# Optimization experiments

Measured on AMD Instinct MI355X. Metric: run time of the kernel, lower is better.

Reference implementation:

```python
import jax, jax.numpy as jnp
import numpy as np

Y_SCALE = 0.01  # fixed weight quantization scale (q_scale of the int8 weights)


def setup_inputs() -> dict:
    key = jax.random.key(0)
    kx, kw, kb = jax.random.split(key, 3)
    B, S, IN, OUT = 4, 2048, 4096, 4096
    x = jax.random.normal(kx, (B, S, IN), dtype=jnp.float32)
    # int8 quantized weights, stored transposed as (in_features, out_features)
    weight_q = jax.random.randint(kw, (IN, OUT), -128, 128, dtype=jnp.int32)
    bias = jax.random.normal(kb, (OUT,), dtype=jnp.float32)
    return {"x": x, "weight_q": weight_q, "bias": bias}


def reference(x, weight_q, bias):
    # Per-batch-sample dynamic activation scale: max(|x_i|)/128 over each [S, IN] slice
    x_scale = jnp.max(jnp.abs(x), axis=(1, 2), keepdims=True) / 128.0  # [B,1,1]
    # int8 quantize: round + clip
    xq = jnp.clip(jnp.round(x / x_scale), -128, 127).astype(jnp.int8)  # [B,S,IN]
    wq = weight_q.astype(jnp.int8)                                      # [IN,OUT]
    c = jax.lax.dot_general(
        xq, wq,
        dimension_numbers=(((2,), (0,)), ((), ())),
        preferred_element_type=jnp.int32,
    )  # [B,S,OUT]
    # dequantize and bias-add
    y = c.astype(jnp.float32) * (x_scale * Y_SCALE)
    return y + bias
```

## Files before the change

kernel.cpp:

```cpp
#include <hip/hip_runtime.h>
#include <stdint.h>

#define K_DIM 4096
#define N_DIM 4096
#define M_DIM 8192
#define S_ROWS 2048
#define NT 32

typedef int v4i __attribute__((ext_vector_type(4)));

__device__ __forceinline__ void gload16(const void* g, void* l) {
    __builtin_amdgcn_global_load_lds(
        (const __attribute__((address_space(1))) unsigned int*)g,
        (__attribute__((address_space(3))) unsigned int*)l, 16, 0, 0);
}

__device__ __forceinline__ void barrier() {
    asm volatile("" ::: "memory");
    __builtin_amdgcn_s_barrier();
    asm volatile("" ::: "memory");
}

__global__ void absmax_kernel(const float* __restrict__ x, unsigned* __restrict__ amax) {
    int b = blockIdx.y;
    const float4* xb = (const float4*)(x + (size_t)b * S_ROWS * K_DIM);
    int tid = blockIdx.x * 256 + threadIdx.x;
    const int stride = 1024 * 256;
    float m = 0.f;
#pragma unroll
    for (int i = 0; i < 8; ++i) {
        float4 v = xb[tid + i * stride];
        m = fmaxf(m, fmaxf(fmaxf(fabsf(v.x), fabsf(v.y)),
                           fmaxf(fabsf(v.z), fabsf(v.w))));
    }
#pragma unroll
    for (int off = 32; off; off >>= 1)
        m = fmaxf(m, __shfl_xor(m, off));
    __shared__ float red[4];
    if ((threadIdx.x & 63) == 0) red[threadIdx.x >> 6] = m;
    __syncthreads();
    if (threadIdx.x == 0) {
        m = fmaxf(fmaxf(red[0], red[1]), fmaxf(red[2], red[3]));
        atomicMax(&amax[b], __float_as_uint(m));
    }
}

__global__ void quant_kernel(const float* __restrict__ x,
                             const unsigned* __restrict__ amax,
                             char* __restrict__ xq) {
    size_t gid = (size_t)blockIdx.x * 256 + threadIdx.x;
    size_t base = gid * 16;
    int b = (int)(base >> 23);
    float inv = 128.0f / __uint_as_float(amax[b]);
    const float4* xs = (const float4*)(x + base);
    unsigned parts[4];
#pragma unroll
    for (int i = 0; i < 4; ++i) {
        float4 v = xs[i];
        int q0 = max(-128, min(127, (int)rintf(v.x * inv)));
        int q1 = max(-128, min(127, (int)rintf(v.y * inv)));
        int q2 = max(-128, min(127, (int)rintf(v.z * inv)));
        int q3 = max(-128, min(127, (int)rintf(v.w * inv)));
        parts[i] = (q0 & 255) | ((q1 & 255) << 8) | ((q2 & 255) << 16) | ((q3 & 255) << 24);
    }
    *(uint4*)(xq + base) = make_uint4(parts[0], parts[1], parts[2], parts[3]);
}

__global__ void wtrans_kernel(const int* __restrict__ wq, char* __restrict__ wt) {
    __shared__ unsigned lds[64 * 17];
    int t = threadIdx.x;
    int c = t & 63;
    int g = t >> 6;
    int n0 = blockIdx.x * 64;
    int k0 = blockIdx.y * 64;
#pragma unroll
    for (int rep = 0; rep < 4; ++rep) {
        int kb = g * 16 + rep * 4;
        int v0 = wq[(size_t)(k0 + kb + 0) * N_DIM + n0 + c];
        int v1 = wq[(size_t)(k0 + kb + 1) * N_DIM + n0 + c];
        int v2 = wq[(size_t)(k0 + kb + 2) * N_DIM + n0 + c];
        int v3 = wq[(size_t)(k0 + kb + 3) * N_DIM + n0 + c];
        lds[c * 17 + (kb >> 2)] =
            (v0 & 255) | ((v1 & 255) << 8) | ((v2 & 255) << 16) | ((v3 & 255) << 24);
    }
    __syncthreads();
    int row = t >> 2;
    int ch = t & 3;
    uint4 o;
    o.x = lds[row * 17 + ch * 4 + 0];
    o.y = lds[row * 17 + ch * 4 + 1];
    o.z = lds[row * 17 + ch * 4 + 2];
    o.w = lds[row * 17 + ch * 4 + 3];
    *(uint4*)(wt + (size_t)(n0 + row) * K_DIM + k0 + ch * 16) = o;
}

__global__ __launch_bounds__(512, 2) void gemm8_kernel(
    const char* __restrict__ A, const char* __restrict__ Bt,
    const float* __restrict__ bias, const unsigned* __restrict__ amax,
    float* __restrict__ out) {
    __shared__ char sm[131072];
    const int t = threadIdx.x;
    const int l = t & 63;
    const int w = t >> 6;
    const int wm = w >> 2;
    const int wn = w & 3;
    const int rb = l & 15;
    const int sg = l >> 4;

    int bid = blockIdx.x;
    int swz = (bid & 7) * 64 + (bid >> 3);
    int mt = swz >> 4, nt = swz & 15;
    const size_t m0 = (size_t)mt * 256;
    const size_t n0 = (size_t)nt * 256;

    v4i acc[8][4];
#pragma unroll
    for (int i = 0; i < 8; ++i)
#pragma unroll
        for (int j = 0; j < 4; ++j) acc[i][j] = (v4i){0, 0, 0, 0};

#define ST_A(tt, h)                                                          \
    if ((tt) < NT) {                                                         \
        char* lb = sm + (((tt) & 1) * 65536);                                \
        const char* gb = A + m0 * K_DIM + (size_t)(tt) * 128;                \
        _Pragma("unroll")                                                    \
        for (int j = 0; j < 2; ++j) {                                        \
            int p = j * 512 + t;                                             \
            int r7 = p >> 3, sl = p & 7;                                     \
            int r = (r7 & 63) + ((r7 >> 6) << 7) + ((h) << 6);               \
            int s = sl ^ (r & 7);                                            \
            gload16(gb + (size_t)r * K_DIM + s * 16, lb + r * 128 + sl * 16);\
        }                                                                    \
    }
#define ST_B(tt, h)                                                          \
    if ((tt) < NT) {                                                         \
        char* lb = sm + (((tt) & 1) * 65536) + 32768;                        \
        const char* gb = Bt + n0 * K_DIM + (size_t)(tt) * 128;               \
        _Pragma("unroll")                                                    \
        for (int j = 0; j < 2; ++j) {                                        \
            int p = j * 512 + t;                                             \
            int r7 = p >> 3, sl = p & 7;                                     \
            int r = ((r7 >> 5) << 6) + ((h) << 5) + (r7 & 31);               \
            int s = sl ^ (r & 7);                                            \
            gload16(gb + (size_t)r * K_DIM + s * 16, lb + r * 128 + sl * 16);\
        }                                                                    \
    }

    ST_A(0, 0); ST_B(0, 0); ST_A(0, 1); ST_B(0, 1); ST_A(1, 0); ST_B(1, 0);

    v4i aF[4][2], bL[2][2], bH[2][2];

    for (int i = 0; i < NT; ++i) {
        const char* pA = sm + (i & 1) * 65536;
        const char* pB = pA + 32768;
        if (i == NT - 1) { asm volatile("s_waitcnt vmcnt(0)" ::: "memory"); }
        else             { asm volatile("s_waitcnt vmcnt(4)" ::: "memory"); }
        barrier();

#pragma unroll
        for (int mi = 0; mi < 4; ++mi)
#pragma unroll
            for (int ks = 0; ks < 2; ++ks) {
                int r = wm * 128 + mi * 16 + rb;
                aF[mi][ks] = *(const v4i*)(pA + r * 128 + (((ks << 2) + sg) ^ (r & 7)) * 16);
            }
#pragma unroll
        for (int ni = 0; ni < 2; ++ni)
#pragma unroll
            for (int ks = 0; ks < 2; ++ks) {
                int r = wn * 64 + ni * 16 + rb;
                bL[ni][ks] = *(const v4i*)(pB + r * 128 + (((ks << 2) + sg) ^ (r & 7)) * 16);
            }
        ST_A(i + 1, 1);
        ST_B(i + 1, 1);
        __builtin_amdgcn_s_setprio(1);
#pragma unroll
        for (int mi = 0; mi < 4; ++mi)
#pragma unroll
            for (int ni = 0; ni < 2; ++ni)
#pragma unroll
                for (int ks = 0; ks < 2; ++ks)
                    acc[mi][ni] = __builtin_amdgcn_mfma_i32_16x16x64_i8(
                        aF[mi][ks], bL[ni][ks], acc[mi][ni], 0, 0, 0);
#pragma unroll
        for (int ni = 0; ni < 2; ++ni)
#pragma unroll
            for (int ks = 0; ks < 2; ++ks) {
                int r = wn * 64 + 32 + ni * 16 + rb;
                bH[ni][ks] = *(const v4i*)(pB + r * 128 + (((ks << 2) + sg) ^ (r & 7)) * 16);
            }
#pragma unroll
        for (int mi = 0; mi < 4; ++mi)
#pragma unroll
            for (int ni = 0; ni < 2; ++ni)
#pragma unroll
                for (int ks = 0; ks < 2; ++ks)
                    acc[mi][ni + 2] = __builtin_amdgcn_mfma_i32_16x16x64_i8(
                        aF[mi][ks], bH[ni][ks], acc[mi][ni + 2], 0, 0, 0);
        __builtin_amdgcn_s_setprio(0);
        barrier();

#pragma unroll
        for (int mi = 0; mi < 4; ++mi)
#pragma unroll
            for (int ks = 0; ks < 2; ++ks) {
                int r = wm * 128 + 64 + mi * 16 + rb;
                aF[mi][ks] = *(const v4i*)(pA + r * 128 + (((ks << 2) + sg) ^ (r & 7)) * 16);
            }
        ST_A(i + 2, 0);
        ST_B(i + 2, 0);
        __builtin_amdgcn_s_setprio(1);
#pragma unroll
        for (int mi = 0; mi < 4; ++mi)
#pragma unroll
            for (int ni = 0; ni < 2; ++ni)
#pragma unroll
                for (int ks = 0; ks < 2; ++ks)
                    acc[mi + 4][ni + 2] = __builtin_amdgcn_mfma_i32_16x16x64_i8(
                        aF[mi][ks], bH[ni][ks], acc[mi + 4][ni + 2], 0, 0, 0);
#pragma unroll
        for (int mi = 0; mi < 4; ++mi)
#pragma unroll
            for (int ni = 0; ni < 2; ++ni)
#pragma unroll
                for (int ks = 0; ks < 2; ++ks)
                    acc[mi + 4][ni] = __builtin_amdgcn_mfma_i32_16x16x64_i8(
                        aF[mi][ks], bL[ni][ks], acc[mi + 4][ni], 0, 0, 0);
        __builtin_amdgcn_s_setprio(0);
    }

    float scale = __uint_as_float(amax[m0 >> 11]) * (1.0f / 128.0f) * 0.01f;
    float bv[4];
#pragma unroll
    for (int ni = 0; ni < 4; ++ni) bv[ni] = bias[n0 + wn * 64 + ni * 16 + rb];
#pragma unroll
    for (int mi = 0; mi < 8; ++mi) {
#pragma unroll
        for (int rg = 0; rg < 4; ++rg) {
            size_t row = m0 + wm * 128 + mi * 16 + sg * 4 + rg;
            float* orow = out + row * N_DIM + n0 + wn * 64 + rb;
#pragma unroll
            for (int ni = 0; ni < 4; ++ni)
                orow[ni * 16] = (float)acc[mi][ni][rg] * scale + bv[ni];
        }
    }
#undef ST_A
#undef ST_B
}

extern "C" void kernel_launch(void* const* d_in, const int* in_sizes, int n_in,
                              void* d_out, int out_size, void* d_ws, size_t ws_size,
                              hipStream_t stream) {
    const float* x = (const float*)d_in[0];
    const int* wq = (const int*)d_in[1];
    const float* bias = (const float*)d_in[2];
    float* out = (float*)d_out;

    unsigned* amax = (unsigned*)d_ws;
    char* xq = (char*)d_ws + 256;
    char* wt = (char*)d_ws + 256 + (size_t)M_DIM * K_DIM;

    hipMemsetAsync(d_ws, 0, 16, stream);

    wtrans_kernel<<<dim3(64, 64), 256, 0, stream>>>(wq, wt);
    absmax_kernel<<<dim3(1024, 4), 256, 0, stream>>>(x, amax);
    quant_kernel<<<8192, 256, 0, stream>>>(x, amax, xq);
    gemm8_kernel<<<dim3(512), 512, 0, stream>>>(xq, wt, bias, amax, out);
}
```

Before: 228.5 us.

## Merge absmax and weight transpose kernels; simplify GEMM to single-stage double buffer

Combines the activation absmax and the weight transpose into one launch, with the block index picking the role, so one kernel launch and its tail gap go away. The GEMM main loop drops the split half-tile prefetch with vmcnt(4) and instead issues a full next-tile load once per iteration behind a vmcnt(0) wait. It also precomputes the swizzled LDS offsets, loads all B fragments at once and removes one barrier per iteration. This cuts barriers and address math, but it weakens the overlap of global loads with compute and holds more fragment registers live.

```diff
diff --git a/kernel.cpp b/kernel.cpp
--- a/kernel.cpp
+++ b/kernel.cpp
@@ -21,27 +21,58 @@
     asm volatile("" ::: "memory");
 }
 
-__global__ void absmax_kernel(const float* __restrict__ x, unsigned* __restrict__ amax) {
-    int b = blockIdx.y;
-    const float4* xb = (const float4*)(x + (size_t)b * S_ROWS * K_DIM);
-    int tid = blockIdx.x * 256 + threadIdx.x;
-    const int stride = 1024 * 256;
-    float m = 0.f;
-#pragma unroll
-    for (int i = 0; i < 8; ++i) {
-        float4 v = xb[tid + i * stride];
-        m = fmaxf(m, fmaxf(fmaxf(fabsf(v.x), fabsf(v.y)),
-                           fmaxf(fabsf(v.z), fabsf(v.w))));
-    }
-#pragma unroll
-    for (int off = 32; off; off >>= 1)
-        m = fmaxf(m, __shfl_xor(m, off));
-    __shared__ float red[4];
-    if ((threadIdx.x & 63) == 0) red[threadIdx.x >> 6] = m;
-    __syncthreads();
-    if (threadIdx.x == 0) {
-        m = fmaxf(fmaxf(red[0], red[1]), fmaxf(red[2], red[3]));
-        atomicMax(&amax[b], __float_as_uint(m));
+__global__ void prep1_kernel(const float* __restrict__ x, unsigned* __restrict__ amax,
+                             const int* __restrict__ wq, char* __restrict__ wt) {
+    __shared__ unsigned lds[64 * 17];
+    if (blockIdx.x < 4096) {
+        int b = blockIdx.x >> 10;
+        int bx = blockIdx.x & 1023;
+        const float4* xb = (const float4*)(x + (size_t)b * S_ROWS * K_DIM);
+        int tid = bx * 256 + threadIdx.x;
+        const int stride = 1024 * 256;
+        float m = 0.f;
+#pragma unroll
+        for (int i = 0; i < 8; ++i) {
+            float4 v = xb[tid + i * stride];
+            m = fmaxf(m, fmaxf(fmaxf(fabsf(v.x), fabsf(v.y)),
+                               fmaxf(fabsf(v.z), fabsf(v.w))));
+        }
+#pragma unroll
+        for (int off = 32; off; off >>= 1)
+            m = fmaxf(m, __shfl_xor(m, off));
+        float* red = (float*)lds;
+        if ((threadIdx.x & 63) == 0) red[threadIdx.x >> 6] = m;
+        __syncthreads();
+        if (threadIdx.x == 0) {
+            m = fmaxf(fmaxf(red[0], red[1]), fmaxf(red[2], red[3]));
+            atomicMax(&amax[b], __float_as_uint(m));
+        }
+    } else {
+        int wb = blockIdx.x - 4096;
+        int n0 = (wb & 63) * 64;
+        int k0 = (wb >> 6) * 64;
+        int t = threadIdx.x;
+        int c = t & 63;
+        int g = t >> 6;
+#pragma unroll
+        for (int rep = 0; rep < 4; ++rep) {
+            int kb = g * 16 + rep * 4;
+            int v0 = wq[(size_t)(k0 + kb + 0) * N_DIM + n0 + c];
+            int v1 = wq[(size_t)(k0 + kb + 1) * N_DIM + n0 + c];
+            int v2 = wq[(size_t)(k0 + kb + 2) * N_DIM + n0 + c];
+            int v3 = wq[(size_t)(k0 + kb + 3) * N_DIM + n0 + c];
+            lds[c * 17 + (kb >> 2)] =
+                (v0 & 255) | ((v1 & 255) << 8) | ((v2 & 255) << 16) | ((v3 & 255) << 24);
+        }
+        __syncthreads();
+        int row = t >> 2;
+        int ch = t & 3;
+        uint4 o;
+        o.x = lds[row * 17 + ch * 4 + 0];
+        o.y = lds[row * 17 + ch * 4 + 1];
+        o.z = lds[row * 17 + ch * 4 + 2];
+        o.w = lds[row * 17 + ch * 4 + 3];
+        *(uint4*)(wt + (size_t)(n0 + row) * K_DIM + k0 + ch * 16) = o;
     }
 }
 
@@ -64,34 +95,6 @@
         parts[i] = (q0 & 255) | ((q1 & 255) << 8) | ((q2 & 255) << 16) | ((q3 & 255) << 24);
     }
     *(uint4*)(xq + base) = make_uint4(parts[0], parts[1], parts[2], parts[3]);
-}
-
-__global__ void wtrans_kernel(const int* __restrict__ wq, char* __restrict__ wt) {
-    __shared__ unsigned lds[64 * 17];
-    int t = threadIdx.x;
-    int c = t & 63;
-    int g = t >> 6;
-    int n0 = blockIdx.x * 64;
-    int k0 = blockIdx.y * 64;
-#pragma unroll
-    for (int rep = 0; rep < 4; ++rep) {
-        int kb = g * 16 + rep * 4;
-        int v0 = wq[(size_t)(k0 + kb + 0) * N_DIM + n0 + c];
-        int v1 = wq[(size_t)(k0 + kb + 1) * N_DIM + n0 + c];
-        int v2 = wq[(size_t)(k0 + kb + 2) * N_DIM + n0 + c];
-        int v3 = wq[(size_t)(k0 + kb + 3) * N_DIM + n0 + c];
-        lds[c * 17 + (kb >> 2)] =
-            (v0 & 255) | ((v1 & 255) << 8) | ((v2 & 255) << 16) | ((v3 & 255) << 24);
-    }
-    __syncthreads();
-    int row = t >> 2;
-    int ch = t & 3;
-    uint4 o;
-    o.x = lds[row * 17 + ch * 4 + 0];
-    o.y = lds[row * 17 + ch * 4 + 1];
-    o.z = lds[row * 17 + ch * 4 + 2];
-    o.w = lds[row * 17 + ch * 4 + 3];
-    *(uint4*)(wt + (size_t)(n0 + row) * K_DIM + k0 + ch * 16) = o;
 }
 
 __global__ __launch_bounds__(512, 2) void gemm8_kernel(
@@ -113,119 +116,87 @@
     const size_t m0 = (size_t)mt * 256;
     const size_t n0 = (size_t)nt * 256;
 
+    const int s0 = (sg ^ (rb & 7)) << 4;
+    const int s1 = s0 ^ 64;
+    const int baseA = (wm * 128 + rb) * 128;
+    const int baseB = 32768 + (wn * 64 + rb) * 128;
+
     v4i acc[8][4];
 #pragma unroll
     for (int i = 0; i < 8; ++i)
 #pragma unroll
         for (int j = 0; j < 4; ++j) acc[i][j] = (v4i){0, 0, 0, 0};
 
-#define ST_A(tt, h)                                                          \
+#define ST_FULL(tt)                                                          \
     if ((tt) < NT) {                                                         \
-        char* lb = sm + (((tt) & 1) * 65536);                                \
-        const char* gb = A + m0 * K_DIM + (size_t)(tt) * 128;                \
-        _Pragma("unroll")                                                    \
-        for (int j = 0; j < 2; ++j) {                                        \
-            int p = j * 512 + t;                                             \
-            int r7 = p >> 3, sl = p & 7;                                     \
-            int r = (r7 & 63) + ((r7 >> 6) << 7) + ((h) << 6);               \
-            int s = sl ^ (r & 7);                                            \
-            gload16(gb + (size_t)r * K_DIM + s * 16, lb + r * 128 + sl * 16);\
-        }                                                                    \
-    }
-#define ST_B(tt, h)                                                          \
-    if ((tt) < NT) {                                                         \
-        char* lb = sm + (((tt) & 1) * 65536) + 32768;                        \
+        char* lb = sm + (((tt) & 1) << 16);                                  \
+        const char* ga = A + m0 * K_DIM + (size_t)(tt) * 128;                \
         const char* gb = Bt + n0 * K_DIM + (size_t)(tt) * 128;               \
         _Pragma("unroll")                                                    \
-        for (int j = 0; j < 2; ++j) {                                        \
+        for (int j = 0; j < 4; ++j) {                                        \
             int p = j * 512 + t;                                             \
-            int r7 = p >> 3, sl = p & 7;                                     \
-            int r = ((r7 >> 5) << 6) + ((h) << 5) + (r7 & 31);               \
+            int r = p >> 3, sl = p & 7;                                      \
             int s = sl ^ (r & 7);                                            \
-            gload16(gb + (size_t)r * K_DIM + s * 16, lb + r * 128 + sl * 16);\
+            gload16(ga + (size_t)r * K_DIM + s * 16, lb + p * 16);           \
         }                                                                    \
-    }
-
-    ST_A(0, 0); ST_B(0, 0); ST_A(0, 1); ST_B(0, 1); ST_A(1, 0); ST_B(1, 0);
-
-    v4i aF[4][2], bL[2][2], bH[2][2];
+        _Pragma("unroll")                                                    \
+        for (int j = 0; j < 4; ++j) {                                        \
+            int p = j * 512 + t;                                             \
+            int r = p >> 3, sl = p & 7;                                      \
+            int s = sl ^ (r & 7);                                            \
+            gload16(gb + (size_t)r * K_DIM + s * 16, lb + 32768 + p * 16);   \
+        }                                                                    \
+    }
+
+    ST_FULL(0);
+
+    v4i aF[4][2], aG[4][2], bF[4][2];
 
     for (int i = 0; i < NT; ++i) {
-        const char* pA = sm + (i & 1) * 65536;
-        const char* pB = pA + 32768;
-        if (i == NT - 1) { asm volatile("s_waitcnt vmcnt(0)" ::: "memory"); }
-        else             { asm volatile("s_waitcnt vmcnt(4)" ::: "memory"); }
+        const char* pb = sm + ((i & 1) << 16);
+        const char* pA0 = pb + baseA + s0;
+        const char* pA1 = pb + baseA + s1;
+        const char* pB0 = pb + baseB + s0;
+        const char* pB1 = pb + baseB + s1;
+
+        asm volatile("s_waitcnt vmcnt(0)" ::: "memory");
         barrier();
 
 #pragma unroll
+        for (int mi = 0; mi < 4; ++mi) {
+            aF[mi][0] = *(const v4i*)(pA0 + mi * 2048);
+            aF[mi][1] = *(const v4i*)(pA1 + mi * 2048);
+        }
+#pragma unroll
+        for (int ni = 0; ni < 4; ++ni) {
+            bF[ni][0] = *(const v4i*)(pB0 + ni * 2048);
+            bF[ni][1] = *(const v4i*)(pB1 + ni * 2048);
+        }
+#pragma unroll
+        for (int mi = 0; mi < 4; ++mi) {
+            aG[mi][0] = *(const v4i*)(pA0 + mi * 2048 + 8192);
+            aG[mi][1] = *(const v4i*)(pA1 + mi * 2048 + 8192);
+        }
+
+        ST_FULL(i + 1);
+
+        __builtin_amdgcn_s_setprio(1);
+#pragma unroll
         for (int mi = 0; mi < 4; ++mi)
 #pragma unroll
-            for (int ks = 0; ks < 2; ++ks) {
-                int r = wm * 128 + mi * 16 + rb;
-                aF[mi][ks] = *(const v4i*)(pA + r * 128 + (((ks << 2) + sg) ^ (r & 7)) * 16);
-            }
-#pragma unroll
-        for (int ni = 0; ni < 2; ++ni)
-#pragma unroll
-            for (int ks = 0; ks < 2; ++ks) {
-                int r = wn * 64 + ni * 16 + rb;
-                bL[ni][ks] = *(const v4i*)(pB + r * 128 + (((ks << 2) + sg) ^ (r & 7)) * 16);
-            }
-        ST_A(i + 1, 1);
-        ST_B(i + 1, 1);
-        __builtin_amdgcn_s_setprio(1);
-#pragma unroll
-        for (int mi = 0; mi < 4; ++mi)
-#pragma unroll
-            for (int ni = 0; ni < 2; ++ni)
+            for (int ni = 0; ni < 4; ++ni)
 #pragma unroll
                 for (int ks = 0; ks < 2; ++ks)
                     acc[mi][ni] = __builtin_amdgcn_mfma_i32_16x16x64_i8(
-                        aF[mi][ks], bL[ni][ks], acc[mi][ni], 0, 0, 0);
-#pragma unroll
-        for (int ni = 0; ni < 2; ++ni)
-#pragma unroll
-            for (int ks = 0; ks < 2; ++ks) {
-                int r = wn * 64 + 32 + ni * 16 + rb;
-                bH[ni][ks] = *(const v4i*)(pB + r * 128 + (((ks << 2) + sg) ^ (r & 7)) * 16);
-            }
+                        aF[mi][ks], bF[ni][ks], acc[mi][ni], 0, 0, 0);
 #pragma unroll
         for (int mi = 0; mi < 4; ++mi)
 #pragma unroll
-            for (int ni = 0; ni < 2; ++ni)
-#pragma unroll
-                for (int ks = 0; ks < 2; ++ks)
-                    acc[mi][ni + 2] = __builtin_amdgcn_mfma_i32_16x16x64_i8(
-                        aF[mi][ks], bH[ni][ks], acc[mi][ni + 2], 0, 0, 0);
-        __builtin_amdgcn_s_setprio(0);
-        barrier();
-
-#pragma unroll
-        for (int mi = 0; mi < 4; ++mi)
-#pragma unroll
-            for (int ks = 0; ks < 2; ++ks) {
-                int r = wm * 128 + 64 + mi * 16 + rb;
-                aF[mi][ks] = *(const v4i*)(pA + r * 128 + (((ks << 2) + sg) ^ (r & 7)) * 16);
-            }
-        ST_A(i + 2, 0);
-        ST_B(i + 2, 0);
-        __builtin_amdgcn_s_setprio(1);
-#pragma unroll
-        for (int mi = 0; mi < 4; ++mi)
-#pragma unroll
-            for (int ni = 0; ni < 2; ++ni)
-#pragma unroll
-                for (int ks = 0; ks < 2; ++ks)
-                    acc[mi + 4][ni + 2] = __builtin_amdgcn_mfma_i32_16x16x64_i8(
-                        aF[mi][ks], bH[ni][ks], acc[mi + 4][ni + 2], 0, 0, 0);
-#pragma unroll
-        for (int mi = 0; mi < 4; ++mi)
-#pragma unroll
-            for (int ni = 0; ni < 2; ++ni)
+            for (int ni = 0; ni < 4; ++ni)
 #pragma unroll
                 for (int ks = 0; ks < 2; ++ks)
                     acc[mi + 4][ni] = __builtin_amdgcn_mfma_i32_16x16x64_i8(
-                        aF[mi][ks], bL[ni][ks], acc[mi + 4][ni], 0, 0, 0);
+                        aG[mi][ks], bF[ni][ks], acc[mi + 4][ni], 0, 0, 0);
         __builtin_amdgcn_s_setprio(0);
     }
 
@@ -244,8 +215,7 @@
                 orow[ni * 16] = (float)acc[mi][ni][rg] * scale + bv[ni];
         }
     }
-#undef ST_A
-#undef ST_B
+#undef ST_FULL
 }
 
 extern "C" void kernel_launch(void* const* d_in, const int* in_sizes, int n_in,
@@ -262,8 +232,7 @@
 
     hipMemsetAsync(d_ws, 0, 16, stream);
 
-    wtrans_kernel<<<dim3(64, 64), 256, 0, stream>>>(wq, wt);
-    absmax_kernel<<<dim3(1024, 4), 256, 0, stream>>>(x, amax);
+    prep1_kernel<<<dim3(8192), 256, 0, stream>>>(x, amax, wq, wt);
     quant_kernel<<<8192, 256, 0, stream>>>(x, amax, xq);
     gemm8_kernel<<<dim3(512), 512, 0, stream>>>(xq, wt, bias, amax, out);
 }
```

Result: faster. 218.5 us (-4.4%).
